# Optimization experiments

Measured on AMD Instinct MI355X. Metric: run time of the kernel, lower is better.

## Reference

```python
import jax, jax.numpy as jnp
import numpy as np

# Protocol constants from NssMPClib config
GELU_TABLE_BIT = 10                      # table_scale_bit
TABLE_SIZE = 2 ** (GELU_TABLE_BIT + 2)   # 4096 entries, covers |x| < 4.0
SCALE_BIT = 16
SCALE = 2 ** SCALE_BIT                   # fixed-point scale of the ring encoding
Y_DIV = SCALE // (2 ** GELU_TABLE_BIT)   # x.scale // 2**table_scale_bit


def setup_inputs() -> dict:
    key = jax.random.key(0)
    # activation tensor (real-valued view of the secret-shared ring tensor)
    x = jax.random.normal(key, (4, 4096, 4096), dtype=jnp.float32)
    # lookup table stores t * Phi(-t) = relu(t) - gelu(t) sampled at t = j / 2^GELU_TABLE_BIT
    j = np.arange(TABLE_SIZE, dtype=np.float64) / (2 ** GELU_TABLE_BIT)
    from scipy.special import erf as _erf_unused  # not available; compute cdf manually
    # standard normal CDF via erf (numpy)
    import math
    phi_neg = 0.5 * (1.0 - np.vectorize(math.erf)(j / math.sqrt(2.0)))
    table = jnp.asarray((j * phi_neg).astype(np.float32))
    return {"x": x, "table": table}


def reference(x, table):
    """Plaintext-equivalent math of the SecGELU CPU protocol.

    Ring semantics: X = round(x * SCALE); y = X // (SCALE // 2^tb);
    d = (y >= 0); a = |y| (via d*y*2 - y); c = a clamped to TABLE_SIZE-1;
    gelu(x) = d*x - table[c]   (table holds relu(t) - gelu(t), an even fn).
    """
    X = jnp.round(x * SCALE)                       # fixed-point ring encode
    y = jnp.floor(X / Y_DIV)                       # ring floor-division
    d = y >= 0
    a = jnp.where(d, y, -y)                        # a = 2*d*y - y = |y|
    c = jnp.where(a < TABLE_SIZE, a, TABLE_SIZE - 1).astype(jnp.int32)
    # d * x  -  LookUp(table, c)
    return jnp.where(d, x, jnp.zeros((), x.dtype)) - table[c]
```

## Files before the change

### kernel.cpp

```cpp
#include <hip/hip_runtime.h>

#define TABLE_SIZE 4096
#define BLOCK 256

typedef float f32x4 __attribute__((ext_vector_type(4)));

__device__ __forceinline__ float secgelu1(float xv, const float* __restrict__ t)
{
    float X = rintf(xv * 65536.0f);
    float y = floorf(X * 0.015625f);
    bool  d = (y >= 0.0f);
    float a = fminf(fabsf(y), (float)(TABLE_SIZE - 1));
    return (d ? xv : 0.0f) - t[(int)a];
}

__global__ __launch_bounds__(BLOCK) void secgelu_kernel(
    const float* __restrict__ x, const float* __restrict__ table,
    float* __restrict__ out, int n4, int n)
{
    __shared__ float lds_table[TABLE_SIZE];
    #pragma unroll
    for (int i = threadIdx.x; i < TABLE_SIZE; i += BLOCK)
        lds_table[i] = table[i];
    __syncthreads();

    const f32x4* __restrict__ x4 = (const f32x4*)x;
    f32x4* __restrict__ o4 = (f32x4*)out;

    const int stride = gridDim.x * BLOCK;
    int idx = blockIdx.x * BLOCK + threadIdx.x;

    for (; idx + stride < n4; idx += 2 * stride) {
        f32x4 v0 = __builtin_nontemporal_load(&x4[idx]);
        f32x4 v1 = __builtin_nontemporal_load(&x4[idx + stride]);
        f32x4 r0, r1;
        #pragma unroll
        for (int k = 0; k < 4; ++k) r0[k] = secgelu1(v0[k], lds_table);
        #pragma unroll
        for (int k = 0; k < 4; ++k) r1[k] = secgelu1(v1[k], lds_table);
        __builtin_nontemporal_store(r0, &o4[idx]);
        __builtin_nontemporal_store(r1, &o4[idx + stride]);
    }
    for (; idx < n4; idx += stride) {
        f32x4 v = __builtin_nontemporal_load(&x4[idx]);
        f32x4 r;
        #pragma unroll
        for (int k = 0; k < 4; ++k) r[k] = secgelu1(v[k], lds_table);
        __builtin_nontemporal_store(r, &o4[idx]);
    }

    int t0 = n4 * 4 + (int)(blockIdx.x * BLOCK + threadIdx.x);
    if (blockIdx.x == 0 && t0 < n) {
        out[t0] = secgelu1(x[t0], lds_table);
    }
}

extern "C" void kernel_launch(void* const* d_in, const int* in_sizes, int n_in,
                              void* d_out, int out_size, void* d_ws, size_t ws_size,
                              hipStream_t stream) {
    const float* x     = (const float*)d_in[0];
    const float* table = (const float*)d_in[1];
    float* out = (float*)d_out;
    int n  = in_sizes[0];
    int n4 = n / 4;

    int blocks = 2048;
    secgelu_kernel<<<blocks, BLOCK, 0, stream>>>(x, table, out, n4, n);
}
```

Before: 430.6 us.

## Software-pipeline input loads with 4-way unroll and overlap table staging

Issues the first batch of four vector loads before copying the lookup table into LDS, so the table fill overlaps the initial global reads. The main loop becomes a register double-buffered pipeline that prefetches the next four vectors while computing and storing the current ones. Input loads switch from nontemporal to regular loads. This raises register use per thread, and the regular loads may change cache behaviour.

```diff
diff --git a/kernel.cpp b/kernel.cpp
--- a/kernel.cpp
+++ b/kernel.cpp
@@ -5,13 +5,19 @@
 
 typedef float f32x4 __attribute__((ext_vector_type(4)));
 
-__device__ __forceinline__ float secgelu1(float xv, const float* __restrict__ t)
+__device__ __forceinline__ f32x4 secgelu4(f32x4 v, const float* __restrict__ t)
 {
-    float X = rintf(xv * 65536.0f);
-    float y = floorf(X * 0.015625f);
-    bool  d = (y >= 0.0f);
-    float a = fminf(fabsf(y), (float)(TABLE_SIZE - 1));
-    return (d ? xv : 0.0f) - t[(int)a];
+    f32x4 r;
+    #pragma unroll
+    for (int k = 0; k < 4; ++k) {
+        float xv = v[k];
+        float X = rintf(xv * 65536.0f);
+        float y = floorf(X * 0.015625f);
+        bool  d = (y >= 0.0f);
+        float a = fminf(fabsf(y), (float)(TABLE_SIZE - 1));
+        r[k] = (d ? xv : 0.0f) - t[(int)a];
+    }
+    return r;
 }
 
 __global__ __launch_bounds__(BLOCK) void secgelu_kernel(
@@ -19,10 +25,6 @@
     float* __restrict__ out, int n4, int n)
 {
     __shared__ float lds_table[TABLE_SIZE];
-    #pragma unroll
-    for (int i = threadIdx.x; i < TABLE_SIZE; i += BLOCK)
-        lds_table[i] = table[i];
-    __syncthreads();
 
     const f32x4* __restrict__ x4 = (const f32x4*)x;
     f32x4* __restrict__ o4 = (f32x4*)out;
@@ -30,28 +32,62 @@
     const int stride = gridDim.x * BLOCK;
     int idx = blockIdx.x * BLOCK + threadIdx.x;
 
-    for (; idx + stride < n4; idx += 2 * stride) {
-        f32x4 v0 = __builtin_nontemporal_load(&x4[idx]);
-        f32x4 v1 = __builtin_nontemporal_load(&x4[idx + stride]);
-        f32x4 r0, r1;
-        #pragma unroll
-        for (int k = 0; k < 4; ++k) r0[k] = secgelu1(v0[k], lds_table);
-        #pragma unroll
-        for (int k = 0; k < 4; ++k) r1[k] = secgelu1(v1[k], lds_table);
-        __builtin_nontemporal_store(r0, &o4[idx]);
-        __builtin_nontemporal_store(r1, &o4[idx + stride]);
+    f32x4 v0, v1, v2, v3;
+    const bool full = (idx + 3 * stride < n4);
+    if (full) {
+        v0 = x4[idx];
+        v1 = x4[idx + stride];
+        v2 = x4[idx + 2 * stride];
+        v3 = x4[idx + 3 * stride];
     }
+
+    #pragma unroll
+    for (int i = threadIdx.x; i < TABLE_SIZE; i += BLOCK)
+        lds_table[i] = table[i];
+    __syncthreads();
+
+    if (full) {
+        for (;;) {
+            int next = idx + 4 * stride;
+            bool more = (next + 3 * stride < n4);
+
+            f32x4 w0, w1, w2, w3;
+            if (more) {
+                w0 = x4[next];
+                w1 = x4[next + stride];
+                w2 = x4[next + 2 * stride];
+                w3 = x4[next + 3 * stride];
+            }
+
+            f32x4 r0 = secgelu4(v0, lds_table);
+            f32x4 r1 = secgelu4(v1, lds_table);
+            f32x4 r2 = secgelu4(v2, lds_table);
+            f32x4 r3 = secgelu4(v3, lds_table);
+
+            __builtin_nontemporal_store(r0, &o4[idx]);
+            __builtin_nontemporal_store(r1, &o4[idx + stride]);
+            __builtin_nontemporal_store(r2, &o4[idx + 2 * stride]);
+            __builtin_nontemporal_store(r3, &o4[idx + 3 * stride]);
+
+            idx = next;
+            if (!more) break;
+            v0 = w0; v1 = w1; v2 = w2; v3 = w3;
+        }
+    }
+
     for (; idx < n4; idx += stride) {
-        f32x4 v = __builtin_nontemporal_load(&x4[idx]);
-        f32x4 r;
-        #pragma unroll
-        for (int k = 0; k < 4; ++k) r[k] = secgelu1(v[k], lds_table);
-        __builtin_nontemporal_store(r, &o4[idx]);
+        f32x4 v = x4[idx];
+        __builtin_nontemporal_store(secgelu4(v, lds_table), &o4[idx]);
     }
 
     int t0 = n4 * 4 + (int)(blockIdx.x * BLOCK + threadIdx.x);
     if (blockIdx.x == 0 && t0 < n) {
-        out[t0] = secgelu1(x[t0], lds_table);
+        float xv = x[t0];
+        float X = rintf(xv * 65536.0f);
+        float y = floorf(X * 0.015625f);
+        bool  d = (y >= 0.0f);
+        float a = fminf(fabsf(y), (float)(TABLE_SIZE - 1));
+        out[t0] = (d ? xv : 0.0f) - lds_table[(int)a];
     }
 }
 
```

After: 474.8 us. 1.1x slower.
